# Performance work log

Hardware: AMD Instinct MI355X
Metric: run time of the kernel (lower is better)

The kernel has to match this reference:

```python
import jax, jax.numpy as jnp
import numpy as np
from jax import lax

B, S, H, V, P = 4, 512, 768, 30522, 512
EPS = 1e-12

def _layer_norm(x, gamma, beta):
    mu = jnp.mean(x, axis=-1, keepdims=True)
    var = jnp.mean(jnp.square(x - mu), axis=-1, keepdims=True)
    return (x - mu) * lax.rsqrt(var + EPS) * gamma + beta

def setup_inputs() -> dict:
    key = jax.random.key(0)
    ks = jax.random.split(key, 8)
    s = 0.02
    hidden_states = jax.random.normal(ks[0], (B, S, H), jnp.float32)
    # values in {-1, 0}; (span_mask > -1) marks in-span positions
    span_mask = jax.random.randint(ks[1], (B, S), -1, 1, dtype=jnp.int64)
    pos_emb = jax.random.normal(ks[2], (P, H), jnp.float32) * s
    W1 = jax.random.normal(ks[3], (3 * H, H), jnp.float32) * s
    b1 = jnp.zeros((H,), jnp.float32)
    g1 = jnp.ones((H,), jnp.float32)
    be1 = jnp.zeros((H,), jnp.float32)
    W2 = jax.random.normal(ks[4], (H, H), jnp.float32) * s
    b2 = jnp.zeros((H,), jnp.float32)
    g2 = jnp.ones((H,), jnp.float32)
    be2 = jnp.zeros((H,), jnp.float32)
    Wdec = jax.random.normal(ks[5], (H, V), jnp.float32) * s
    dec_bias = jnp.zeros((V,), jnp.float32)
    return {"hidden_states": hidden_states, "span_mask": span_mask, "pos_emb": pos_emb,
            "W1": W1, "b1": b1, "g1": g1, "be1": be1,
            "W2": W2, "b2": b2, "g2": g2, "be2": be2,
            "Wdec": Wdec, "dec_bias": dec_bias}

def reference(hidden_states, span_mask, pos_emb, W1, b1, g1, be1, W2, b2, g2, be2, Wdec, dec_bias):
    mask = span_mask > -1                       # [B,S] bool
    idx = jnp.arange(S, dtype=jnp.int64)
    # position embeddings via default position_ids = arange(S)
    pe = jnp.broadcast_to(pos_emb[:S][None], (B, S, H))
    # fw recurrence: fw[j] = j-1 if (mask[j] & ~mask[j-1]) else fw[j-1]; fw[0]=0
    prev = jnp.pad(mask[:, :-1], ((0, 0), (1, 0)))
    start = mask & ~prev & (idx > 0)[None]
    c_fw = jnp.where(start, idx - 1, 0)
    fw = lax.cummax(c_fw, axis=1)               # last span-start index (parallel max-scan)
    # bw recurrence: bw[j] = j+1 if (mask[j] & ~mask[j+1]) else bw[j+1]; bw[S-1]=S-1
    nxt = jnp.pad(mask[:, 1:], ((0, 0), (0, 1)))
    end = mask & ~nxt & (idx < S - 1)[None]
    c_bw = jnp.where(end, idx + 1, S - 1)
    bw = lax.cummin(c_bw, axis=1, reverse=True)  # nearest span-end index (reverse min-scan)
    fw_h = jnp.take_along_axis(hidden_states, fw[:, :, None], axis=1)  # [B,S,H]
    bw_h = jnp.take_along_axis(hidden_states, bw[:, :, None], axis=1)
    sbo = jnp.concatenate([fw_h, bw_h, pe], axis=-1)                   # [B,S,3H]
    sbo = sbo * mask[:, :, None].astype(sbo.dtype)
    mid = _layer_norm(jax.nn.gelu(sbo @ W1 + b1, approximate=False).astype(jnp.float32), g1, be1)
    pre = _layer_norm(jax.nn.gelu(mid @ W2 + b2, approximate=False).astype(jnp.float32), g2, be2)
    logits = pre @ Wdec + dec_bias                                     # [B,S,V]
    return logits
```

## Files before the change

### kernel.cpp

```cpp
#include <hip/hip_runtime.h>
#include <hip/hip_bf16.h>

#define BSZ 4
#define SEQ 512
#define HID 768
#define VOC 30522
#define NPAD 30720

typedef __attribute__((ext_vector_type(8))) short short8;
typedef __attribute__((ext_vector_type(4))) float f32x4;

typedef const unsigned int __attribute__((address_space(1)))* gptr_t;
typedef unsigned int __attribute__((address_space(3)))* lptr_t;

__device__ __forceinline__ void gload_lds16(const void* g, void* l) {
    __builtin_amdgcn_global_load_lds((gptr_t)g, (lptr_t)l, 16, 0, 0);
}

__global__ __launch_bounds__(512) void scan_kernel(const int* __restrict__ span,
                                                   int* __restrict__ fw, int* __restrict__ bw) {
    int b = blockIdx.x;
    int j = threadIdx.x;
    __shared__ int sm[SEQ];
    __shared__ int sc[SEQ];
    int m = (span[b * SEQ + j] > -1) ? 1 : 0;
    sm[j] = m;
    __syncthreads();
    int prev = (j > 0) ? sm[j - 1] : 0;
    int nxt  = (j < SEQ - 1) ? sm[j + 1] : 0;
    int cfw = (m && !prev && j > 0) ? (j - 1) : 0;
    int cbw = (m && !nxt && j < SEQ - 1) ? (j + 1) : (SEQ - 1);

    int v = cfw;
    sc[j] = v; __syncthreads();
    for (int off = 1; off < SEQ; off <<= 1) {
        int o = (j >= off) ? sc[j - off] : 0;
        __syncthreads();
        v = max(v, o);
        sc[j] = v; __syncthreads();
    }
    fw[b * SEQ + j] = v;

    v = cbw;
    sc[j] = v; __syncthreads();
    for (int off = 1; off < SEQ; off <<= 1) {
        int o = (j + off < SEQ) ? sc[j + off] : (SEQ - 1);
        __syncthreads();
        v = min(v, o);
        sc[j] = v; __syncthreads();
    }
    bw[b * SEQ + j] = v;
}

__global__ __launch_bounds__(384) void build_x(const float* __restrict__ h,
                                               const int* __restrict__ span,
                                               const float* __restrict__ pe,
                                               const int* __restrict__ fw,
                                               const int* __restrict__ bw,
                                               __hip_bfloat16* __restrict__ X) {
    int r = blockIdx.x;
    int b = r >> 9, s = r & (SEQ - 1);
    float mf = (span[r] > -1) ? 1.f : 0.f;
    int f = fw[r], w = bw[r];
    const float* hf = h + ((size_t)b * SEQ + f) * HID;
    const float* hb = h + ((size_t)b * SEQ + w) * HID;
    const float* pp = pe + (size_t)s * HID;
    __hip_bfloat16* xr = X + (size_t)r * (3 * HID);
    int c = threadIdx.x * 2;
    #pragma unroll
    for (int seg = 0; seg < 3; seg++) {
        const float* src = (seg == 0) ? hf : (seg == 1) ? hb : pp;
        float2 v = *(const float2*)&src[c];
        __hip_bfloat16 lo = __float2bfloat16(v.x * mf);
        __hip_bfloat16 hi = __float2bfloat16(v.y * mf);
        unsigned int pk = ((unsigned int)*(unsigned short*)&hi << 16) | *(unsigned short*)&lo;
        *(unsigned int*)&xr[seg * HID + c] = pk;
    }
}

#define T1_TILES (12 * 36)
#define T2_TILES (12 * 12)
#define TD_TILES (480 * 12)
__global__ __launch_bounds__(256) void transpose_all(const float* __restrict__ W1, __hip_bfloat16* __restrict__ W1t,
                                                     const float* __restrict__ W2, __hip_bfloat16* __restrict__ W2t,
                                                     const float* __restrict__ Wd, __hip_bfloat16* __restrict__ Wdt) {
    int flat = blockIdx.x;
    const float* W; __hip_bfloat16* Wt; int K, N, tx_tiles, idx;
    if (flat < T1_TILES)                { W = W1; Wt = W1t; K = 3 * HID; N = HID; tx_tiles = 12;  idx = flat; }
    else if (flat < T1_TILES + T2_TILES){ W = W2; Wt = W2t; K = HID;     N = HID; tx_tiles = 12;  idx = flat - T1_TILES; }
    else                                { W = Wd; Wt = Wdt; K = HID;     N = VOC; tx_tiles = 480; idx = flat - T1_TILES - T2_TILES; }
    int n0 = (idx % tx_tiles) * 64, k0 = (idx / tx_tiles) * 64;

    __shared__ float t[64][67];
    int tx = threadIdx.x & 31, ty = threadIdx.x >> 5;
    #pragma unroll
    for (int i = 0; i < 64; i += 8) {
        #pragma unroll
        for (int jx = 0; jx < 64; jx += 32) {
            int k = k0 + ty + i, n = n0 + tx + jx;
            t[ty + i][tx + jx] = (n < N) ? W[(size_t)k * N + n] : 0.f;
        }
    }
    __syncthreads();
    #pragma unroll
    for (int i = 0; i < 8; i++) {
        int nn = ty + i * 8;
        int n = n0 + nn;
        float a = t[tx * 2][nn], b = t[tx * 2 + 1][nn];
        __hip_bfloat16 ba = __float2bfloat16(a), bb = __float2bfloat16(b);
        unsigned int pk = ((unsigned int)*(unsigned short*)&bb << 16) | *(unsigned short*)&ba;
        *(unsigned int*)&Wt[(size_t)n * K + k0 + tx * 2] = pk;
    }
}

template<int P>
__global__ __launch_bounds__(256) void gelu_ln(const float* __restrict__ Y, size_t ystride,
                                               const float* __restrict__ bias,
                                               const float* __restrict__ g,
                                               const float* __restrict__ be,
                                               __hip_bfloat16* __restrict__ out) {
    int r = blockIdx.x;
    float z[3];
    float s1 = 0.f, s2 = 0.f;
    #pragma unroll
    for (int i = 0; i < 3; i++) {
        int c = threadIdx.x + i * 256;
        float x = bias[c];
        #pragma unroll
        for (int p = 0; p < P; p++)
            x += Y[p * ystride + (size_t)r * HID + c];
        float zz = 0.5f * x * (1.f + erff(x * 0.70710678118654752f));
        z[i] = zz; s1 += zz; s2 += zz * zz;
    }
    #pragma unroll
    for (int off = 32; off; off >>= 1) {
        s1 += __shfl_down(s1, off);
        s2 += __shfl_down(s2, off);
    }
    __shared__ float p1[4], p2[4];
    int w = threadIdx.x >> 6, lane = threadIdx.x & 63;
    if (lane == 0) { p1[w] = s1; p2[w] = s2; }
    __syncthreads();
    s1 = p1[0] + p1[1] + p1[2] + p1[3];
    s2 = p2[0] + p2[1] + p2[2] + p2[3];
    float mu = s1 * (1.f / HID);
    float var = s2 * (1.f / HID) - mu * mu;
    float rs = rsqrtf(var + 1e-12f);
    __hip_bfloat16* o = out + (size_t)r * HID;
    #pragma unroll
    for (int i = 0; i < 3; i++) {
        int c = threadIdx.x + i * 256;
        o[c] = __float2bfloat16((z[i] - mu) * rs * g[c] + be[c]);
    }
}

__global__ __launch_bounds__(256) void gemm_splitk(const __hip_bfloat16* __restrict__ A,
                                                   const __hip_bfloat16* __restrict__ Bt,
                                                   float* __restrict__ C,
                                                   int lda, int Klen, int ldc, size_t cstride) {
    __shared__ __hip_bfloat16 As[128 * 64];
    __shared__ __hip_bfloat16 Bs[128 * 64];
    int bx = blockIdx.x;
    int by = blockIdx.y;
    int koff = blockIdx.z * Klen;
    float* Cz = C + (size_t)blockIdx.z * cstride;
    int t = threadIdx.x;
    int lane = t & 63, w = t >> 6;
    int wm = w >> 1, wn = w & 1;

    const __hip_bfloat16* Ab = A + (size_t)(by * 128) * lda + koff;
    const __hip_bfloat16* Bb = Bt + (size_t)(bx * 128) * lda + koff;

    f32x4 acc[4][4] = {};

    for (int k0 = 0; k0 < Klen; k0 += 64) {
        #pragma unroll
        for (int i = 0; i < 4; i++) {
            int c = i * 256 + t;
            int row = c >> 3, col = (c & 7) * 8;
            gload_lds16(Ab + (size_t)row * lda + k0 + col, (char*)As + c * 16);
            gload_lds16(Bb + (size_t)row * lda + k0 + col, (char*)Bs + c * 16);
        }
        __syncthreads();
        #pragma unroll
        for (int kk = 0; kk < 64; kk += 32) {
            short8 a[4], b[4];
            int col = kk + (lane >> 4) * 8;
            #pragma unroll
            for (int mi = 0; mi < 4; mi++) {
                int row = wm * 64 + mi * 16 + (lane & 15);
                a[mi] = *(const short8*)&As[row * 64 + col];
            }
            #pragma unroll
            for (int ni = 0; ni < 4; ni++) {
                int row = wn * 64 + ni * 16 + (lane & 15);
                b[ni] = *(const short8*)&Bs[row * 64 + col];
            }
            #pragma unroll
            for (int mi = 0; mi < 4; mi++)
                #pragma unroll
                for (int ni = 0; ni < 4; ni++)
                    acc[mi][ni] = __builtin_amdgcn_mfma_f32_16x16x32_bf16(a[mi], b[ni], acc[mi][ni], 0, 0, 0);
        }
        __syncthreads();
    }

    int rq = lane >> 4, cl = lane & 15;
    #pragma unroll
    for (int mi = 0; mi < 4; mi++) {
        #pragma unroll
        for (int ni = 0; ni < 4; ni++) {
            int col = bx * 128 + wn * 64 + ni * 16 + cl;
            #pragma unroll
            for (int j = 0; j < 4; j++) {
                int row = by * 128 + wm * 64 + mi * 16 + rq * 4 + j;
                Cz[(size_t)row * ldc + col] = acc[mi][ni][j];
            }
        }
    }
}

#define KTILES 12
#define TPB 4
#define VTOT (KTILES * TPB)
__global__ __launch_bounds__(512, 2) void gemm256p(const __hip_bfloat16* __restrict__ A,
                                                   const __hip_bfloat16* __restrict__ Bt,
                                                   float* __restrict__ C,
                                                   int K, int Nvalid,
                                                   const float* __restrict__ bias, int ldc) {
    __shared__ char lds[131072];
    int h = blockIdx.x;
    int chunk = gridDim.x >> 3;
    int l = (h & 7) * chunk + (h >> 3);
    int bn = l >> 1;
    int bm0 = (l & 1) * 4;

    int tid = threadIdx.x;
    int lane = tid & 63;
    int w = tid >> 6;
    int wr = w >> 2, wc = w & 3;

    int r0 = tid >> 3;
    int swz8 = (((tid & 7) ^ (r0 & 7)) << 3);
    const __hip_bfloat16* Bbase = Bt + (size_t)(bn * 256) * K;
    size_t arow0 = (size_t)r0 * K + swz8;
    size_t arow1 = arow0 + (size_t)64 * K;
    int ldsw = tid * 16;

    int rxor = (lane & 7) << 4;
    int rcol = ((lane >> 4) & 3) * 16;
    int rc0 = (0 + rcol) ^ rxor;
    int rc1 = (64 + rcol) ^ rxor;
    int aoff = (wr * 64 + (lane & 15)) * 128;
    int boff = 32768 + (wc * 32 + (lane & 15)) * 128;

    int rq = lane >> 4, cl = lane & 15;
    float bv[2][2];
    #pragma unroll
    for (int qn = 0; qn < 2; qn++)
        #pragma unroll
        for (int ni = 0; ni < 2; ni++) {
            int col = bn * 256 + qn * 128 + wc * 32 + ni * 16 + cl;
            bv[qn][ni] = (col < Nvalid) ? bias[col] : 0.f;
        }

    f32x4 acc[2][2][4][2] = {};

#define ABASE(va) (A + (size_t)((bm0 + (va) / KTILES) * 256) * K)
#define KKOF(va)  (((va) % KTILES) * 64)
#define STAGEA(va, half) do { \
        const __hip_bfloat16* gg = ABASE(va) + (size_t)(half) * 128 * K + KKOF(va); \
        char* dd = lds + ((va) & 1) * 65536 + (half) * 16384 + ldsw; \
        gload_lds16(gg + arow0, dd); \
        gload_lds16(gg + arow1, dd + 8192); } while (0)
#define STAGEB(va, half) do { \
        const __hip_bfloat16* gg = Bbase + (size_t)(half) * 128 * K + KKOF(va); \
        char* dd = lds + ((va) & 1) * 65536 + 32768 + (half) * 16384 + ldsw; \
        gload_lds16(gg + arow0, dd); \
        gload_lds16(gg + arow1, dd + 8192); } while (0)

#define MFMA_Q(qm, qn, AF, BF) do { \
        _Pragma("unroll") \
        for (int mi = 0; mi < 4; mi++) \
            _Pragma("unroll") \
            for (int ni = 0; ni < 2; ni++) { \
                acc[qm][qn][mi][ni] = __builtin_amdgcn_mfma_f32_16x16x32_bf16(AF[mi][0], BF[ni][0], acc[qm][qn][mi][ni], 0, 0, 0); \
                acc[qm][qn][mi][ni] = __builtin_amdgcn_mfma_f32_16x16x32_bf16(AF[mi][1], BF[ni][1], acc[qm][qn][mi][ni], 0, 0, 0); \
            } } while (0)

#define WRQ(qm, qn) do { \
        int bmw = bm0 + v / KTILES; \
        _Pragma("unroll") \
        for (int mi = 0; mi < 4; mi++) \
            _Pragma("unroll") \
            for (int ni = 0; ni < 2; ni++) { \
                int col = bn * 256 + (qn) * 128 + wc * 32 + ni * 16 + cl; \
                if (col < Nvalid) { \
                    _Pragma("unroll") \
                    for (int j = 0; j < 4; j++) { \
                        int row = bmw * 256 + (qm) * 128 + wr * 64 + mi * 16 + rq * 4 + j; \
                        C[(size_t)row * ldc + col] = acc[qm][qn][mi][ni][j] + bv[qn][ni]; \
                    } \
                } \
                acc[qm][qn][mi][ni] = (f32x4){0.f, 0.f, 0.f, 0.f}; \
            } } while (0)

#define BAR() __builtin_amdgcn_s_barrier()

    STAGEA(0, 0); STAGEB(0, 0); STAGEB(0, 1); STAGEA(0, 1);
    STAGEA(1, 0); STAGEB(1, 0); STAGEB(1, 1);
    asm volatile("s_waitcnt vmcnt(6)" ::: "memory");
    BAR();

    short8 af0[4][2], af1[4][2], bf0[2][2], bf1[2][2];
    for (int v = 0; v < VTOT; ++v) {
        int d = (v & 1) * 65536;
        bool last = ((v % KTILES) == KTILES - 1);

        #pragma unroll
        for (int mi = 0; mi < 4; mi++) {
            af0[mi][0] = *(const short8*)(lds + d + aoff + mi * 2048 + rc0);
            af0[mi][1] = *(const short8*)(lds + d + aoff + mi * 2048 + rc1);
        }
        #pragma unroll
        for (int ni = 0; ni < 2; ni++) {
            bf0[ni][0] = *(const short8*)(lds + d + boff + ni * 2048 + rc0);
            bf0[ni][1] = *(const short8*)(lds + d + boff + ni * 2048 + rc1);
            bf1[ni][0] = *(const short8*)(lds + d + boff + 16384 + ni * 2048 + rc0);
            bf1[ni][1] = *(const short8*)(lds + d + boff + 16384 + ni * 2048 + rc1);
        }
        #pragma unroll
        for (int mi = 0; mi < 4; mi++) {
            af1[mi][0] = *(const short8*)(lds + d + 16384 + aoff + mi * 2048 + rc0);
            af1[mi][1] = *(const short8*)(lds + d + 16384 + aoff + mi * 2048 + rc1);
        }
        if (v + 1 < VTOT) STAGEA(v + 1, 1);
        BAR();
        __builtin_amdgcn_s_setprio(1);
        MFMA_Q(0, 0, af0, bf0);
        MFMA_Q(0, 1, af0, bf1);
        __builtin_amdgcn_s_setprio(0);
        if (last) { WRQ(0, 0); WRQ(0, 1); }

        if (v + 2 < VTOT) { STAGEA(v + 2, 0); STAGEB(v + 2, 0); STAGEB(v + 2, 1); }
        if (v < VTOT - 2) asm volatile("s_waitcnt vmcnt(6)" ::: "memory");
        else              asm volatile("s_waitcnt vmcnt(0)" ::: "memory");
        BAR();
        __builtin_amdgcn_s_setprio(1);
        MFMA_Q(1, 1, af1, bf1);
        MFMA_Q(1, 0, af1, bf0);
        __builtin_amdgcn_s_setprio(0);
        if (last) { WRQ(1, 1); WRQ(1, 0); }
    }
#undef STAGEA
#undef STAGEB
#undef MFMA_Q
#undef WRQ
#undef BAR
#undef ABASE
#undef KKOF
}

extern "C" void kernel_launch(void* const* d_in, const int* in_sizes, int n_in,
                              void* d_out, int out_size, void* d_ws, size_t ws_size,
                              hipStream_t stream) {
    const float* hidden = (const float*)d_in[0];
    const int*   span   = (const int*)d_in[1];
    const float* pe     = (const float*)d_in[2];
    const float* W1     = (const float*)d_in[3];
    const float* b1     = (const float*)d_in[4];
    const float* g1     = (const float*)d_in[5];
    const float* be1    = (const float*)d_in[6];
    const float* W2     = (const float*)d_in[7];
    const float* b2     = (const float*)d_in[8];
    const float* g2     = (const float*)d_in[9];
    const float* be2    = (const float*)d_in[10];
    const float* Wdec   = (const float*)d_in[11];
    const float* dbias  = (const float*)d_in[12];
    float* out = (float*)d_out;

    const int M = BSZ * SEQ;
    char* ws = (char*)d_ws;
    size_t off = 0;
    int* fw = (int*)(ws + off);                 off += (size_t)M * 4;
    int* bw = (int*)(ws + off);                 off += (size_t)M * 4;
    __hip_bfloat16* Xb   = (__hip_bfloat16*)(ws + off); off += (size_t)M * 3 * HID * 2;
    __hip_bfloat16* W1t  = (__hip_bfloat16*)(ws + off); off += (size_t)HID * 3 * HID * 2;
    __hip_bfloat16* W2t  = (__hip_bfloat16*)(ws + off); off += (size_t)HID * HID * 2;
    __hip_bfloat16* Wdt  = (__hip_bfloat16*)(ws + off); off += (size_t)NPAD * HID * 2;
    float* Y             = (float*)(ws + off);          off += (size_t)M * HID * 4 * 4;
    __hip_bfloat16* mid  = (__hip_bfloat16*)(ws + off); off += (size_t)M * HID * 2;
    __hip_bfloat16* pre  = (__hip_bfloat16*)(ws + off); off += (size_t)M * HID * 2;
    size_t ystride = (size_t)M * HID;

    scan_kernel<<<BSZ, SEQ, 0, stream>>>(span, fw, bw);
    build_x<<<M, 384, 0, stream>>>(hidden, span, pe, fw, bw, Xb);
    transpose_all<<<T1_TILES + T2_TILES + TD_TILES, 256, 0, stream>>>(W1, W1t, W2, W2t, Wdec, Wdt);
    gemm_splitk<<<dim3(HID / 128, M / 128, 4), 256, 0, stream>>>(Xb, W1t, Y, 3 * HID, 3 * HID / 4, HID, ystride);
    gelu_ln<4><<<M, 256, 0, stream>>>(Y, ystride, b1, g1, be1, mid);
    gemm_splitk<<<dim3(HID / 128, M / 128, 2), 256, 0, stream>>>(mid, W2t, Y, HID, HID / 2, HID, ystride);
    gelu_ln<2><<<M, 256, 0, stream>>>(Y, ystride, b2, g2, be2, pre);
    gemm256p<<<240, 512, 0, stream>>>(pre, Wdt, out, HID, VOC, dbias, VOC);
}
```

Measured before the change: 218.0 us.

## Shrink decoder GEMM tiles to 128x128 with 256-thread persistent blocks

```diff
diff --git a/kernel.cpp b/kernel.cpp
--- a/kernel.cpp
+++ b/kernel.cpp
@@ -221,141 +221,133 @@
 }
 
 #define KTILES 12
-#define TPB 4
+#define TPB 8
 #define VTOT (KTILES * TPB)
-__global__ __launch_bounds__(512, 2) void gemm256p(const __hip_bfloat16* __restrict__ A,
+__global__ __launch_bounds__(256, 2) void gemm128p(const __hip_bfloat16* __restrict__ A,
                                                    const __hip_bfloat16* __restrict__ Bt,
                                                    float* __restrict__ C,
                                                    int K, int Nvalid,
                                                    const float* __restrict__ bias, int ldc) {
-    __shared__ char lds[131072];
+    __shared__ char lds[65536];
     int h = blockIdx.x;
     int chunk = gridDim.x >> 3;
     int l = (h & 7) * chunk + (h >> 3);
     int bn = l >> 1;
-    int bm0 = (l & 1) * 4;
+    int bm0 = (l & 1) * TPB;
 
     int tid = threadIdx.x;
     int lane = tid & 63;
     int w = tid >> 6;
-    int wr = w >> 2, wc = w & 3;
+    int wr = w >> 1, wc = w & 1;
 
     int r0 = tid >> 3;
     int swz8 = (((tid & 7) ^ (r0 & 7)) << 3);
-    const __hip_bfloat16* Bbase = Bt + (size_t)(bn * 256) * K;
-    size_t arow0 = (size_t)r0 * K + swz8;
-    size_t arow1 = arow0 + (size_t)64 * K;
+    const __hip_bfloat16* Bbase = Bt + (size_t)(bn * 128) * K;
+    size_t arow = (size_t)r0 * K + swz8;
     int ldsw = tid * 16;
 
     int rxor = (lane & 7) << 4;
-    int rcol = ((lane >> 4) & 3) * 16;
-    int rc0 = (0 + rcol) ^ rxor;
+    int rcol = (lane >> 4) * 16;
+    int rc0 = rcol ^ rxor;
     int rc1 = (64 + rcol) ^ rxor;
     int aoff = (wr * 64 + (lane & 15)) * 128;
-    int boff = 32768 + (wc * 32 + (lane & 15)) * 128;
+    int boff = 16384 + (wc * 64 + (lane & 15)) * 128;
 
     int rq = lane >> 4, cl = lane & 15;
-    float bv[2][2];
-    #pragma unroll
-    for (int qn = 0; qn < 2; qn++)
-        #pragma unroll
-        for (int ni = 0; ni < 2; ni++) {
-            int col = bn * 256 + qn * 128 + wc * 32 + ni * 16 + cl;
-            bv[qn][ni] = (col < Nvalid) ? bias[col] : 0.f;
-        }
-
-    f32x4 acc[2][2][4][2] = {};
-
-#define ABASE(va) (A + (size_t)((bm0 + (va) / KTILES) * 256) * K)
+    float bv[4];
+    #pragma unroll
+    for (int ni = 0; ni < 4; ni++) {
+        int col = bn * 128 + wc * 64 + ni * 16 + cl;
+        bv[ni] = (col < Nvalid) ? bias[col] : 0.f;
+    }
+
+    f32x4 acc[4][4] = {};
+
+#define ABASE(va) (A + (size_t)((bm0 + (va) / KTILES) * 128) * K)
 #define KKOF(va)  (((va) % KTILES) * 64)
-#define STAGEA(va, half) do { \
-        const __hip_bfloat16* gg = ABASE(va) + (size_t)(half) * 128 * K + KKOF(va); \
-        char* dd = lds + ((va) & 1) * 65536 + (half) * 16384 + ldsw; \
-        gload_lds16(gg + arow0, dd); \
-        gload_lds16(gg + arow1, dd + 8192); } while (0)
-#define STAGEB(va, half) do { \
-        const __hip_bfloat16* gg = Bbase + (size_t)(half) * 128 * K + KKOF(va); \
-        char* dd = lds + ((va) & 1) * 65536 + 32768 + (half) * 16384 + ldsw; \
-        gload_lds16(gg + arow0, dd); \
-        gload_lds16(gg + arow1, dd + 8192); } while (0)
-
-#define MFMA_Q(qm, qn, AF, BF) do { \
+#define STQ1(va) do { const __hip_bfloat16* gg = ABASE(va) + KKOF(va); \
+        char* dd = lds + ((va) & 1) * 32768 + ldsw; \
+        gload_lds16(gg + arow, dd); gload_lds16(gg + arow + (size_t)32 * K, dd + 4096); } while (0)
+#define STQ2(va) do { const __hip_bfloat16* gg = ABASE(va) + KKOF(va) + (size_t)64 * K; \
+        char* dd = lds + ((va) & 1) * 32768 + 8192 + ldsw; \
+        gload_lds16(gg + arow, dd); gload_lds16(gg + arow + (size_t)32 * K, dd + 4096); } while (0)
+#define STQ3(va) do { const __hip_bfloat16* gg = Bbase + KKOF(va); \
+        char* dd = lds + ((va) & 1) * 32768 + 16384 + ldsw; \
+        gload_lds16(gg + arow, dd); gload_lds16(gg + arow + (size_t)32 * K, dd + 4096); } while (0)
+#define STQ4(va) do { const __hip_bfloat16* gg = Bbase + KKOF(va) + (size_t)64 * K; \
+        char* dd = lds + ((va) & 1) * 32768 + 24576 + ldsw; \
+        gload_lds16(gg + arow, dd); gload_lds16(gg + arow + (size_t)32 * K, dd + 4096); } while (0)
+
+#define MFMA_N(n0) do { \
         _Pragma("unroll") \
         for (int mi = 0; mi < 4; mi++) \
             _Pragma("unroll") \
-            for (int ni = 0; ni < 2; ni++) { \
-                acc[qm][qn][mi][ni] = __builtin_amdgcn_mfma_f32_16x16x32_bf16(AF[mi][0], BF[ni][0], acc[qm][qn][mi][ni], 0, 0, 0); \
-                acc[qm][qn][mi][ni] = __builtin_amdgcn_mfma_f32_16x16x32_bf16(AF[mi][1], BF[ni][1], acc[qm][qn][mi][ni], 0, 0, 0); \
+            for (int nn = (n0); nn < (n0) + 2; nn++) { \
+                acc[mi][nn] = __builtin_amdgcn_mfma_f32_16x16x32_bf16(af[mi][0], bf[nn][0], acc[mi][nn], 0, 0, 0); \
+                acc[mi][nn] = __builtin_amdgcn_mfma_f32_16x16x32_bf16(af[mi][1], bf[nn][1], acc[mi][nn], 0, 0, 0); \
             } } while (0)
 
-#define WRQ(qm, qn) do { \
+#define WRN(n0) do { \
         int bmw = bm0 + v / KTILES; \
         _Pragma("unroll") \
         for (int mi = 0; mi < 4; mi++) \
             _Pragma("unroll") \
-            for (int ni = 0; ni < 2; ni++) { \
-                int col = bn * 256 + (qn) * 128 + wc * 32 + ni * 16 + cl; \
+            for (int nn = (n0); nn < (n0) + 2; nn++) { \
+                int col = bn * 128 + wc * 64 + nn * 16 + cl; \
                 if (col < Nvalid) { \
                     _Pragma("unroll") \
                     for (int j = 0; j < 4; j++) { \
-                        int row = bmw * 256 + (qm) * 128 + wr * 64 + mi * 16 + rq * 4 + j; \
-                        C[(size_t)row * ldc + col] = acc[qm][qn][mi][ni][j] + bv[qn][ni]; \
+                        int row = bmw * 128 + wr * 64 + mi * 16 + rq * 4 + j; \
+                        C[(size_t)row * ldc + col] = acc[mi][nn][j] + bv[nn]; \
                     } \
                 } \
-                acc[qm][qn][mi][ni] = (f32x4){0.f, 0.f, 0.f, 0.f}; \
+                acc[mi][nn] = (f32x4){0.f, 0.f, 0.f, 0.f}; \
             } } while (0)
 
 #define BAR() __builtin_amdgcn_s_barrier()
 
-    STAGEA(0, 0); STAGEB(0, 0); STAGEB(0, 1); STAGEA(0, 1);
-    STAGEA(1, 0); STAGEB(1, 0); STAGEB(1, 1);
+    STQ1(0); STQ2(0); STQ3(0); STQ4(0);
+    STQ2(1); STQ3(1); STQ4(1);
     asm volatile("s_waitcnt vmcnt(6)" ::: "memory");
     BAR();
 
-    short8 af0[4][2], af1[4][2], bf0[2][2], bf1[2][2];
+    short8 af[4][2], bf[4][2];
     for (int v = 0; v < VTOT; ++v) {
-        int d = (v & 1) * 65536;
+        int d = (v & 1) * 32768;
         bool last = ((v % KTILES) == KTILES - 1);
 
         #pragma unroll
         for (int mi = 0; mi < 4; mi++) {
-            af0[mi][0] = *(const short8*)(lds + d + aoff + mi * 2048 + rc0);
-            af0[mi][1] = *(const short8*)(lds + d + aoff + mi * 2048 + rc1);
-        }
-        #pragma unroll
-        for (int ni = 0; ni < 2; ni++) {
-            bf0[ni][0] = *(const short8*)(lds + d + boff + ni * 2048 + rc0);
-            bf0[ni][1] = *(const short8*)(lds + d + boff + ni * 2048 + rc1);
-            bf1[ni][0] = *(const short8*)(lds + d + boff + 16384 + ni * 2048 + rc0);
-            bf1[ni][1] = *(const short8*)(lds + d + boff + 16384 + ni * 2048 + rc1);
-        }
-        #pragma unroll
-        for (int mi = 0; mi < 4; mi++) {
-            af1[mi][0] = *(const short8*)(lds + d + 16384 + aoff + mi * 2048 + rc0);
-            af1[mi][1] = *(const short8*)(lds + d + 16384 + aoff + mi * 2048 + rc1);
-        }
-        if (v + 1 < VTOT) STAGEA(v + 1, 1);
+            af[mi][0] = *(const short8*)(lds + d + aoff + mi * 2048 + rc0);
+            af[mi][1] = *(const short8*)(lds + d + aoff + mi * 2048 + rc1);
+        }
+        #pragma unroll
+        for (int ni = 0; ni < 4; ni++) {
+            bf[ni][0] = *(const short8*)(lds + d + boff + ni * 2048 + rc0);
+            bf[ni][1] = *(const short8*)(lds + d + boff + ni * 2048 + rc1);
+        }
+        if (v + 1 < VTOT) STQ1(v + 1);
         BAR();
         __builtin_amdgcn_s_setprio(1);
-        MFMA_Q(0, 0, af0, bf0);
-        MFMA_Q(0, 1, af0, bf1);
+        MFMA_N(0);
         __builtin_amdgcn_s_setprio(0);
-        if (last) { WRQ(0, 0); WRQ(0, 1); }
-
-        if (v + 2 < VTOT) { STAGEA(v + 2, 0); STAGEB(v + 2, 0); STAGEB(v + 2, 1); }
+        if (last) WRN(0);
+
+        if (v + 2 < VTOT) { STQ2(v + 2); STQ3(v + 2); STQ4(v + 2); }
         if (v < VTOT - 2) asm volatile("s_waitcnt vmcnt(6)" ::: "memory");
         else              asm volatile("s_waitcnt vmcnt(0)" ::: "memory");
         BAR();
         __builtin_amdgcn_s_setprio(1);
-        MFMA_Q(1, 1, af1, bf1);
-        MFMA_Q(1, 0, af1, bf0);
+        MFMA_N(2);
         __builtin_amdgcn_s_setprio(0);
-        if (last) { WRQ(1, 1); WRQ(1, 0); }
-    }
-#undef STAGEA
-#undef STAGEB
-#undef MFMA_Q
-#undef WRQ
+        if (last) WRN(2);
+    }
+#undef STQ1
+#undef STQ2
+#undef STQ3
+#undef STQ4
+#undef MFMA_N
+#undef WRN
 #undef BAR
 #undef ABASE
 #undef KKOF
@@ -400,5 +392,5 @@
     gelu_ln<4><<<M, 256, 0, stream>>>(Y, ystride, b1, g1, be1, mid);
     gemm_splitk<<<dim3(HID / 128, M / 128, 2), 256, 0, stream>>>(mid, W2t, Y, HID, HID / 2, HID, ystride);
     gelu_ln<2><<<M, 256, 0, stream>>>(Y, ystride, b2, g2, be2, pre);
-    gemm256p<<<240, 512, 0, stream>>>(pre, Wdt, out, HID, VOC, dbias, VOC);
-}
+    gemm128p<<<480, 256, 0, stream>>>(pre, Wdt, out, HID, VOC, dbias, VOC);
+}
```

Result: slower. 259.0 us (+18.8%).

## Double-buffer split-K GEMM with swizzled LDS and staged async prefetch

Applied to the files above, without the earlier changes.

```diff
diff --git a/kernel.cpp b/kernel.cpp
--- a/kernel.cpp
+++ b/kernel.cpp
@@ -154,55 +154,91 @@
     }
 }
 
-__global__ __launch_bounds__(256) void gemm_splitk(const __hip_bfloat16* __restrict__ A,
-                                                   const __hip_bfloat16* __restrict__ Bt,
-                                                   float* __restrict__ C,
-                                                   int lda, int Klen, int ldc, size_t cstride) {
-    __shared__ __hip_bfloat16 As[128 * 64];
-    __shared__ __hip_bfloat16 Bs[128 * 64];
-    int bx = blockIdx.x;
-    int by = blockIdx.y;
+__global__ __launch_bounds__(256, 2) void gemm_splitk(const __hip_bfloat16* __restrict__ A,
+                                                      const __hip_bfloat16* __restrict__ Bt,
+                                                      float* __restrict__ C,
+                                                      int lda, int Klen, int ldc, size_t cstride) {
+    __shared__ char lds[65536];
+    int bx = blockIdx.x, by = blockIdx.y;
     int koff = blockIdx.z * Klen;
     float* Cz = C + (size_t)blockIdx.z * cstride;
-    int t = threadIdx.x;
-    int lane = t & 63, w = t >> 6;
-    int wm = w >> 1, wn = w & 1;
-
-    const __hip_bfloat16* Ab = A + (size_t)(by * 128) * lda + koff;
-    const __hip_bfloat16* Bb = Bt + (size_t)(bx * 128) * lda + koff;
+
+    int tid = threadIdx.x;
+    int lane = tid & 63;
+    int w = tid >> 6;
+    int wr = w >> 1, wc = w & 1;
+
+    int r0 = tid >> 3;
+    int swz8 = (((tid & 7) ^ (r0 & 7)) << 3);
+    const __hip_bfloat16* Abase = A + (size_t)(by * 128) * lda + koff;
+    const __hip_bfloat16* Bbase = Bt + (size_t)(bx * 128) * lda + koff;
+    size_t arow = (size_t)r0 * lda + swz8;
+    int ldsw = tid * 16;
+
+    int rxor = (lane & 7) << 4;
+    int rcol = (lane >> 4) * 16;
+    int rc0 = rcol ^ rxor;
+    int rc1 = (64 + rcol) ^ rxor;
+    int aoff = (wr * 64 + (lane & 15)) * 128;
+    int boff = 16384 + (wc * 64 + (lane & 15)) * 128;
 
     f32x4 acc[4][4] = {};
-
-    for (int k0 = 0; k0 < Klen; k0 += 64) {
-        #pragma unroll
-        for (int i = 0; i < 4; i++) {
-            int c = i * 256 + t;
-            int row = c >> 3, col = (c & 7) * 8;
-            gload_lds16(Ab + (size_t)row * lda + k0 + col, (char*)As + c * 16);
-            gload_lds16(Bb + (size_t)row * lda + k0 + col, (char*)Bs + c * 16);
-        }
-        __syncthreads();
-        #pragma unroll
-        for (int kk = 0; kk < 64; kk += 32) {
-            short8 a[4], b[4];
-            int col = kk + (lane >> 4) * 8;
-            #pragma unroll
-            for (int mi = 0; mi < 4; mi++) {
-                int row = wm * 64 + mi * 16 + (lane & 15);
-                a[mi] = *(const short8*)&As[row * 64 + col];
-            }
-            #pragma unroll
-            for (int ni = 0; ni < 4; ni++) {
-                int row = wn * 64 + ni * 16 + (lane & 15);
-                b[ni] = *(const short8*)&Bs[row * 64 + col];
-            }
-            #pragma unroll
-            for (int mi = 0; mi < 4; mi++)
-                #pragma unroll
-                for (int ni = 0; ni < 4; ni++)
-                    acc[mi][ni] = __builtin_amdgcn_mfma_f32_16x16x32_bf16(a[mi], b[ni], acc[mi][ni], 0, 0, 0);
-        }
-        __syncthreads();
+    int nt = Klen >> 6;
+
+#define STQ1(t) do { const __hip_bfloat16* gg = Abase + (t) * 64; \
+        char* dd = lds + ((t) & 1) * 32768 + ldsw; \
+        gload_lds16(gg + arow, dd); gload_lds16(gg + arow + (size_t)32 * lda, dd + 4096); } while (0)
+#define STQ2(t) do { const __hip_bfloat16* gg = Abase + (t) * 64 + (size_t)64 * lda; \
+        char* dd = lds + ((t) & 1) * 32768 + 8192 + ldsw; \
+        gload_lds16(gg + arow, dd); gload_lds16(gg + arow + (size_t)32 * lda, dd + 4096); } while (0)
+#define STQ3(t) do { const __hip_bfloat16* gg = Bbase + (t) * 64; \
+        char* dd = lds + ((t) & 1) * 32768 + 16384 + ldsw; \
+        gload_lds16(gg + arow, dd); gload_lds16(gg + arow + (size_t)32 * lda, dd + 4096); } while (0)
+#define STQ4(t) do { const __hip_bfloat16* gg = Bbase + (t) * 64 + (size_t)64 * lda; \
+        char* dd = lds + ((t) & 1) * 32768 + 24576 + ldsw; \
+        gload_lds16(gg + arow, dd); gload_lds16(gg + arow + (size_t)32 * lda, dd + 4096); } while (0)
+
+#define MFMA_N(n0) do { \
+        _Pragma("unroll") \
+        for (int mi = 0; mi < 4; mi++) \
+            _Pragma("unroll") \
+            for (int nn = (n0); nn < (n0) + 2; nn++) { \
+                acc[mi][nn] = __builtin_amdgcn_mfma_f32_16x16x32_bf16(af[mi][0], bf[nn][0], acc[mi][nn], 0, 0, 0); \
+                acc[mi][nn] = __builtin_amdgcn_mfma_f32_16x16x32_bf16(af[mi][1], bf[nn][1], acc[mi][nn], 0, 0, 0); \
+            } } while (0)
+
+    STQ1(0); STQ2(0); STQ3(0); STQ4(0);
+    STQ2(1); STQ3(1); STQ4(1);
+    asm volatile("s_waitcnt vmcnt(6)" ::: "memory");
+    __builtin_amdgcn_s_barrier();
+
+    short8 af[4][2], bf[4][2];
+    for (int t = 0; t < nt; ++t) {
+        int d = (t & 1) * 32768;
+
+        #pragma unroll
+        for (int mi = 0; mi < 4; mi++) {
+            af[mi][0] = *(const short8*)(lds + d + aoff + mi * 2048 + rc0);
+            af[mi][1] = *(const short8*)(lds + d + aoff + mi * 2048 + rc1);
+        }
+        #pragma unroll
+        for (int ni = 0; ni < 4; ni++) {
+            bf[ni][0] = *(const short8*)(lds + d + boff + ni * 2048 + rc0);
+            bf[ni][1] = *(const short8*)(lds + d + boff + ni * 2048 + rc1);
+        }
+        if (t + 1 < nt) STQ1(t + 1);
+        __builtin_amdgcn_s_barrier();
+        __builtin_amdgcn_s_setprio(1);
+        MFMA_N(0);
+        __builtin_amdgcn_s_setprio(0);
+
+        if (t + 2 < nt) { STQ2(t + 2); STQ3(t + 2); STQ4(t + 2); }
+        if (t < nt - 2) asm volatile("s_waitcnt vmcnt(6)" ::: "memory");
+        else            asm volatile("s_waitcnt vmcnt(0)" ::: "memory");
+        __builtin_amdgcn_s_barrier();
+        __builtin_amdgcn_s_setprio(1);
+        MFMA_N(2);
+        __builtin_amdgcn_s_setprio(0);
     }
 
     int rq = lane >> 4, cl = lane & 15;
@@ -210,14 +246,19 @@
     for (int mi = 0; mi < 4; mi++) {
         #pragma unroll
         for (int ni = 0; ni < 4; ni++) {
-            int col = bx * 128 + wn * 64 + ni * 16 + cl;
+            int col = bx * 128 + wc * 64 + ni * 16 + cl;
             #pragma unroll
             for (int j = 0; j < 4; j++) {
-                int row = by * 128 + wm * 64 + mi * 16 + rq * 4 + j;
+                int row = by * 128 + wr * 64 + mi * 16 + rq * 4 + j;
                 Cz[(size_t)row * ldc + col] = acc[mi][ni][j];
             }
         }
     }
+#undef STQ1
+#undef STQ2
+#undef STQ3
+#undef STQ4
+#undef MFMA_N
 }
 
 #define KTILES 12
```

Measured after the change: 210.8 us. 3.3% less time.
